# Performance work log

Hardware: AMD Instinct MI355X
Metric: run time of the kernel (lower is better)

## Reference

```python
import jax, jax.numpy as jnp
import numpy as np

B, U, D, SKIP = 2048, 1024, 1024, 24

def setup_inputs() -> dict:
    key = jax.random.key(0)
    ks = jax.random.split(key, 8)
    return {
        "inputs": jax.random.normal(ks[0], (B, D), dtype=jnp.float32),
        "h_tm1": jax.random.normal(ks[1], (B, 4 * U), dtype=jnp.float32),
        "c_tm1": jax.random.normal(ks[2], (B, U), dtype=jnp.float32),
        "step": jnp.zeros((B, 1), dtype=jnp.float32),
        "prev_h": jax.random.normal(ks[3], (B, U * SKIP), dtype=jnp.float32),
        "kernel": jax.random.normal(ks[4], (D, 4 * U), dtype=jnp.float32) * (1.0 / np.sqrt(D)),
        "recurrent_kernel": jax.random.normal(ks[5], (U, 4 * U), dtype=jnp.float32) * (1.0 / np.sqrt(U)),
        "kernel2": jax.random.normal(ks[6], (U, U), dtype=jnp.float32) * (1.0 / np.sqrt(U)),
        "bias": jnp.zeros((4 * U,), dtype=jnp.float32),
        "bias2": jnp.zeros((U,), dtype=jnp.float32),
        "s0": jnp.float32(0.5),
    }

def reference(inputs, h_tm1, c_tm1, step, prev_h, kernel, recurrent_kernel, kernel2, bias, bias2, s0):
    units = kernel2.shape[0]
    # split previous 'h' state into its four gate-history blocks [B, U] each
    h_parts = jnp.stack(jnp.split(h_tm1, 4, axis=1), axis=0)          # [4, B, U]
    rk = recurrent_kernel.reshape(units, 4, units)                     # [U, 4, U]
    # fused per-gate recurrent matmuls: r[g] = h_parts[g] @ recurrent_kernel[:, g*U:(g+1)*U]
    r = jnp.einsum('gbu,ugv->gbv', h_parts, rk)                        # [4, B, U]
    x = inputs @ kernel + bias                                         # [B, 4U]
    x_i, x_f, x_c, x_o = jnp.split(x, 4, axis=1)
    i = jax.nn.sigmoid(x_i + r[0])
    f = jax.nn.sigmoid(x_f + r[1])
    c = f * c_tm1 + i * jnp.tanh(x_c + r[2])
    o = jax.nn.sigmoid(x_o + r[3])
    h = o * jnp.tanh(c)
    new_h_skip = jax.nn.sigmoid(prev_h[:, :units] @ kernel2 + bias2)
    h = s0 * h + new_h_skip * (1 - s0)
    new_h_tm1 = jnp.concatenate([i, f, c, o], axis=1)
    new_prev_h = jnp.concatenate([prev_h[:, units:], h], axis=1)
    return (h, new_h_tm1, c, step + 1, new_prev_h)
```

## Files before the change

kernel.cpp:

```cpp
#include <hip/hip_runtime.h>
#include <hip/hip_bf16.h>
#include <stdint.h>

#define BB 2048
#define UU 1024
#define SKIPN 24

typedef __attribute__((ext_vector_type(8))) short short8;
typedef __attribute__((ext_vector_type(4))) float f32x4;
typedef __attribute__((ext_vector_type(4))) unsigned short ushort4_t;

static __device__ __forceinline__ float sigmoidf_(float x) {
    return 1.0f / (1.0f + __expf(-x));
}

static __device__ __forceinline__ void load_lds16(const void* g, void* l) {
    __builtin_amdgcn_global_load_lds((const __attribute__((address_space(1))) void*)g,
                                     (__attribute__((address_space(3))) void*)l, 16, 0, 0);
}

__global__ __launch_bounds__(256) void prep(
    const float* __restrict__ inputs, const float* __restrict__ h_tm1,
    const float* __restrict__ prev_h, const float* __restrict__ kernel,
    const float* __restrict__ rkernel, const float* __restrict__ kernel2,
    __hip_bfloat16* __restrict__ kt, __hip_bfloat16* __restrict__ rkt,
    __hip_bfloat16* __restrict__ k2t, __hip_bfloat16* __restrict__ xin,
    __hip_bfloat16* __restrict__ hb, __hip_bfloat16* __restrict__ ph0) {
    const int bid = blockIdx.x;
    if (bid < 9216) {
        __shared__ float tile[32][33];
        const float* src;
        __hip_bfloat16* dst;
        int C, local;
        if (bid < 4096)      { src = kernel;  dst = kt;  C = 4096; local = bid; }
        else if (bid < 8192) { src = rkernel; dst = rkt; C = 4096; local = bid - 4096; }
        else                 { src = kernel2; dst = k2t; C = 1024; local = bid - 8192; }
        const int xt = (C == 4096) ? 128 : 32;
        const int bc = (local % xt) * 32;
        const int br = (local / xt) * 32;
        const int tx = threadIdx.x & 31, ty = threadIdx.x >> 5;
#pragma unroll
        for (int i = 0; i < 32; i += 8)
            tile[ty + i][tx] = src[(size_t)(br + ty + i) * C + bc + tx];
        __syncthreads();
#pragma unroll
        for (int i = 0; i < 32; i += 8)
            dst[(size_t)(bc + ty + i) * 1024 + br + tx] = __float2bfloat16(tile[tx][ty + i]);
    } else {
        const int idx = (bid - 9216) * 256 + threadIdx.x;
        const float* src;
        __hip_bfloat16* dst;
        int off;
        if (idx < 524288) { dst = xin; off = idx; src = inputs + (size_t)off * 4; }
        else if (idx < 2621440) { off = idx - 524288; dst = hb; src = h_tm1 + (size_t)off * 4; }
        else {
            const int i = idx - 2621440;
            const int b = i >> 8, c4 = i & 255;
            off = i; dst = ph0;
            src = prev_h + (size_t)b * (UU * SKIPN) + c4 * 4;
        }
        const float4 v = *(const float4*)src;
        union { __hip_bfloat16 h[4]; ushort4_t u; } cv;
        cv.h[0] = __float2bfloat16(v.x);
        cv.h[1] = __float2bfloat16(v.y);
        cv.h[2] = __float2bfloat16(v.z);
        cv.h[3] = __float2bfloat16(v.w);
        *(ushort4_t*)(dst + (size_t)off * 4) = cv.u;
    }
}

__global__ __launch_bounds__(256) void mega3(
    const __hip_bfloat16* __restrict__ xin,
    const __hip_bfloat16* __restrict__ hb,
    const __hip_bfloat16* __restrict__ ph0,
    const __hip_bfloat16* __restrict__ kt,
    const __hip_bfloat16* __restrict__ rkt,
    const __hip_bfloat16* __restrict__ k2t,
    const float* __restrict__ prev_h, float* __restrict__ out_prev,
    float* __restrict__ pre) {
    const int bid = blockIdx.x;
    if (bid >= 640) {
        const int b = bid - 640;
        const float4* s = (const float4*)(prev_h + (size_t)b * 24576 + 1024);
        float4* d = (float4*)(out_prev + (size_t)b * 24576);
        for (int c = threadIdx.x; c < 5888; c += 256) d[c] = s[c];
        return;
    }
    const int gi = bid;
    const int g = gi % 5;
    const int t = gi / 5;
    const int v0 = (t & 7) * 128;
    const int b0 = (t >> 3) * 128;

    __shared__ short As[128 * 32];
    __shared__ short Bs[128 * 32];

    const int tid = threadIdx.x;
    const int lane = tid & 63;
    const int wid = tid >> 6;
    const int wrow = wid >> 1;
    const int wcol = wid & 1;

    const int srow = tid >> 2;
    const int sslot = tid & 3;
    const int kofs = ((sslot ^ (srow & 3)) << 3);
    char* dA = (char*)As + wid * 1024;
    char* dB = (char*)Bs + wid * 1024;

    const int l15 = lane & 15;
    const int hi = lane >> 4;
    const int rswB = ((hi ^ (l15 & 3)) << 4);

    f32x4 acc[4][4];
#pragma unroll
    for (int m = 0; m < 4; m++)
#pragma unroll
        for (int n = 0; n < 4; n++) acc[m][n] = (f32x4){0.f, 0.f, 0.f, 0.f};

    const __hip_bfloat16* A1;
    const __hip_bfloat16* W1;
    const __hip_bfloat16* A2 = nullptr;
    const __hip_bfloat16* W2 = nullptr;
    int lda1;
    if (g < 4) {
        A1 = xin; lda1 = 1024;
        W1 = kt + (size_t)g * 1048576;
        A2 = hb + (size_t)g * 1024;
        W2 = rkt + (size_t)g * 1048576;
    } else {
        A1 = ph0; lda1 = 1024;
        W1 = k2t;
    }

#define KSEG(AB, LDA, WB)                                                          \
    {                                                                              \
        const __hip_bfloat16* Ar0 = (AB) + (size_t)(b0 + srow) * (LDA) + kofs;     \
        const __hip_bfloat16* Ar1 = (AB) + (size_t)(b0 + 64 + srow) * (LDA) + kofs;\
        const __hip_bfloat16* Wr0 = (WB) + (size_t)(v0 + srow) * 1024 + kofs;      \
        const __hip_bfloat16* Wr1 = (WB) + (size_t)(v0 + 64 + srow) * 1024 + kofs; \
        for (int k0 = 0; k0 < 1024; k0 += 32) {                                    \
            load_lds16(Ar0 + k0, dA);                                              \
            load_lds16(Ar1 + k0, dA + 4096);                                       \
            load_lds16(Wr0 + k0, dB);                                              \
            load_lds16(Wr1 + k0, dB + 4096);                                       \
            __syncthreads();                                                       \
            short8 af[4], bfr[4];                                                  \
            _Pragma("unroll")                                                      \
            for (int m = 0; m < 4; m++)                                            \
                af[m] = *(const short8*)((char*)As + (wrow * 64 + m * 16 + l15) * 64 + rswB); \
            _Pragma("unroll")                                                      \
            for (int n = 0; n < 4; n++)                                            \
                bfr[n] = *(const short8*)((char*)Bs + (wcol * 64 + n * 16 + l15) * 64 + rswB); \
            _Pragma("unroll")                                                      \
            for (int m = 0; m < 4; m++)                                            \
                _Pragma("unroll")                                                  \
                for (int n = 0; n < 4; n++)                                        \
                    acc[m][n] = __builtin_amdgcn_mfma_f32_16x16x32_bf16(af[m], bfr[n], acc[m][n], 0, 0, 0); \
            __syncthreads();                                                       \
        }                                                                          \
    }

    KSEG(A1, lda1, W1);
    if (g < 4) KSEG(A2, 4096, W2);
#undef KSEG

    float* P = pre + (size_t)g * 2097152;
#pragma unroll
    for (int m = 0; m < 4; m++) {
#pragma unroll
        for (int n = 0; n < 4; n++) {
            const int col = v0 + wcol * 64 + n * 16 + l15;
            const int row = b0 + wrow * 64 + m * 16 + hi * 4;
#pragma unroll
            for (int r = 0; r < 4; r++)
                P[(size_t)(row + r) * 1024 + col] = acc[m][n][r];
        }
    }
}

__global__ __launch_bounds__(256) void epilogue2(
    const float* __restrict__ pre,
    const float* __restrict__ c_tm1, const float* __restrict__ bias,
    const float* __restrict__ bias2, const float* __restrict__ s0p,
    const float* __restrict__ step, float* __restrict__ out_h,
    float* __restrict__ out_ht, float* __restrict__ out_c,
    float* __restrict__ out_step, float* __restrict__ out_prev, int write_tail) {
    const int idx = blockIdx.x * 256 + threadIdx.x;
    const int b = idx >> 8;
    const int v = (idx & 255) * 4;
    const size_t bv = (size_t)b * 1024 + v;
    const float4 pi = *(const float4*)(pre + bv);
    const float4 pf = *(const float4*)(pre + 2097152 + bv);
    const float4 pc = *(const float4*)(pre + 4194304 + bv);
    const float4 po = *(const float4*)(pre + 6291456 + bv);
    const float4 ps = *(const float4*)(pre + 8388608 + bv);
    const float4 ct = *(const float4*)(c_tm1 + bv);
    const float4 bi = *(const float4*)(bias + v);
    const float4 bf_ = *(const float4*)(bias + 1024 + v);
    const float4 bc = *(const float4*)(bias + 2048 + v);
    const float4 bo = *(const float4*)(bias + 3072 + v);
    const float4 b2 = *(const float4*)(bias2 + v);
    const float s0 = s0p[0];

    float4 hv, iv4, fv4, cn4, ov4;
#pragma unroll
    for (int j = 0; j < 4; j++) {
        const float iv = sigmoidf_(((const float*)&pi)[j] + ((const float*)&bi)[j]);
        const float fv = sigmoidf_(((const float*)&pf)[j] + ((const float*)&bf_)[j]);
        const float cn = fv * ((const float*)&ct)[j] + iv * tanhf(((const float*)&pc)[j] + ((const float*)&bc)[j]);
        const float ov = sigmoidf_(((const float*)&po)[j] + ((const float*)&bo)[j]);
        const float sk = sigmoidf_(((const float*)&ps)[j] + ((const float*)&b2)[j]);
        ((float*)&hv)[j] = s0 * (ov * tanhf(cn)) + sk * (1.0f - s0);
        ((float*)&iv4)[j] = iv;
        ((float*)&fv4)[j] = fv;
        ((float*)&cn4)[j] = cn;
        ((float*)&ov4)[j] = ov;
    }
    *(float4*)(out_h + bv) = hv;
    *(float4*)(out_c + bv) = cn4;
    float* ht = out_ht + (size_t)b * 4096 + v;
    *(float4*)(ht) = iv4;
    *(float4*)(ht + 1024) = fv4;
    *(float4*)(ht + 2048) = cn4;
    *(float4*)(ht + 3072) = ov4;
    if (write_tail)
        *(float4*)(out_prev + (size_t)b * 24576 + 23552 + v) = hv;
    if (idx < 2048) out_step[idx] = step[idx] + 1.0f;
}

__global__ __launch_bounds__(256) void shift_only(
    const float* __restrict__ prev_h, const float* __restrict__ out_h,
    float* __restrict__ out_prev) {
    const int b = blockIdx.x;
    float4* d = (float4*)(out_prev + (size_t)b * 24576);
    const float4* s1 = (const float4*)(prev_h + (size_t)b * 24576 + 1024);
    const float4* s2 = (const float4*)(out_h + (size_t)b * 1024);
    for (int c = threadIdx.x; c < 6144; c += 256)
        d[c] = (c < 5888) ? s1[c] : s2[c - 5888];
}

extern "C" void kernel_launch(void* const* d_in, const int* in_sizes, int n_in,
                              void* d_out, int out_size, void* d_ws, size_t ws_size,
                              hipStream_t stream) {
    (void)in_sizes; (void)n_in; (void)out_size;
    const float* inputs = (const float*)d_in[0];
    const float* h_tm1 = (const float*)d_in[1];
    const float* c_tm1 = (const float*)d_in[2];
    const float* step = (const float*)d_in[3];
    const float* prev_h = (const float*)d_in[4];
    const float* kernel = (const float*)d_in[5];
    const float* rkernel = (const float*)d_in[6];
    const float* kernel2 = (const float*)d_in[7];
    const float* bias = (const float*)d_in[8];
    const float* bias2 = (const float*)d_in[9];
    const float* s0 = (const float*)d_in[10];

    float* out = (float*)d_out;
    float* out_h = out;
    float* out_ht = out + 2097152;
    float* out_c = out + 10485760;
    float* out_step = out + 12582912;
    float* out_prev = out + 12584960;

    const size_t NEED = 44040192 + 41943040;
    const int fits = (ws_size >= NEED);
    char* scr = fits ? (char*)d_ws : (char*)out_prev;
    __hip_bfloat16* kt = (__hip_bfloat16*)(scr + 0);
    __hip_bfloat16* rkt = (__hip_bfloat16*)(scr + 8388608);
    __hip_bfloat16* k2t = (__hip_bfloat16*)(scr + 16777216);
    __hip_bfloat16* xin = (__hip_bfloat16*)(scr + 18874368);
    __hip_bfloat16* hb = (__hip_bfloat16*)(scr + 23068672);
    __hip_bfloat16* ph0 = (__hip_bfloat16*)(scr + 39845888);
    float* pre = (float*)(scr + 44040192);

    prep<<<21504, 256, 0, stream>>>(inputs, h_tm1, prev_h, kernel, rkernel, kernel2,
                                    kt, rkt, k2t, xin, hb, ph0);
    if (fits) {
        mega3<<<2688, 256, 0, stream>>>(xin, hb, ph0, kt, rkt, k2t, prev_h, out_prev, pre);
        epilogue2<<<2048, 256, 0, stream>>>(pre, c_tm1, bias, bias2, s0, step,
                                            out_h, out_ht, out_c, out_step, out_prev, 1);
    } else {
        mega3<<<640, 256, 0, stream>>>(xin, hb, ph0, kt, rkt, k2t, prev_h, out_prev, pre);
        epilogue2<<<2048, 256, 0, stream>>>(pre, c_tm1, bias, bias2, s0, step,
                                            out_h, out_ht, out_c, out_step, out_prev, 0);
        shift_only<<<2048, 256, 0, stream>>>(prev_h, out_h, out_prev);
    }
}
```

Measured before the change: 196.8 us.

## Double-buffer LDS tiles in GEMM kernel and use nontemporal copy for prev_h shift

The GEMM main loop now uses two LDS buffers, issuing the next k-tile's global-to-LDS loads before computing on the current tile. It replaces __syncthreads with explicit vmcnt/lgkmcnt waits and raw s_barrier so memory latency can overlap with MFMA work. The prev_h shift-copy blocks switch to unrolled nontemporal loads and stores to avoid polluting the cache. LDS use doubles, which may reduce occupancy, and the hand-placed waitcnts are fragile.

```diff
diff --git a/kernel.cpp b/kernel.cpp
--- a/kernel.cpp
+++ b/kernel.cpp
@@ -17,6 +17,13 @@
 static __device__ __forceinline__ void load_lds16(const void* g, void* l) {
     __builtin_amdgcn_global_load_lds((const __attribute__((address_space(1))) void*)g,
                                      (__attribute__((address_space(3))) void*)l, 16, 0, 0);
+}
+
+static __device__ __forceinline__ f32x4 ntl(const f32x4* p) {
+    return __builtin_nontemporal_load(p);
+}
+static __device__ __forceinline__ void nts(f32x4* p, f32x4 v) {
+    __builtin_nontemporal_store(v, p);
 }
 
 __global__ __launch_bounds__(256) void prep(
@@ -69,7 +76,7 @@
     }
 }
 
-__global__ __launch_bounds__(256) void mega3(
+__global__ __launch_bounds__(256) void mega4(
     const __hip_bfloat16* __restrict__ xin,
     const __hip_bfloat16* __restrict__ hb,
     const __hip_bfloat16* __restrict__ ph0,
@@ -81,9 +88,29 @@
     const int bid = blockIdx.x;
     if (bid >= 640) {
         const int b = bid - 640;
-        const float4* s = (const float4*)(prev_h + (size_t)b * 24576 + 1024);
-        float4* d = (float4*)(out_prev + (size_t)b * 24576);
-        for (int c = threadIdx.x; c < 5888; c += 256) d[c] = s[c];
+        const f32x4* s = (const f32x4*)(prev_h + (size_t)b * 24576 + 1024);
+        f32x4* d = (f32x4*)(out_prev + (size_t)b * 24576);
+        int c = threadIdx.x;
+#pragma unroll 1
+        for (int it = 0; it < 5; ++it) {
+            f32x4 v0 = ntl(s + c);
+            f32x4 v1 = ntl(s + c + 256);
+            f32x4 v2 = ntl(s + c + 512);
+            f32x4 v3 = ntl(s + c + 768);
+            nts(d + c, v0);
+            nts(d + c + 256, v1);
+            nts(d + c + 512, v2);
+            nts(d + c + 768, v3);
+            c += 1024;
+        }
+        {
+            f32x4 v0 = ntl(s + c);
+            f32x4 v1 = ntl(s + c + 256);
+            f32x4 v2 = ntl(s + c + 512);
+            nts(d + c, v0);
+            nts(d + c + 256, v1);
+            nts(d + c + 512, v2);
+        }
         return;
     }
     const int gi = bid;
@@ -92,8 +119,8 @@
     const int v0 = (t & 7) * 128;
     const int b0 = (t >> 3) * 128;
 
-    __shared__ short As[128 * 32];
-    __shared__ short Bs[128 * 32];
+    __shared__ char As[2 * 8192];
+    __shared__ char Bs[2 * 8192];
 
     const int tid = threadIdx.x;
     const int lane = tid & 63;
@@ -104,8 +131,7 @@
     const int srow = tid >> 2;
     const int sslot = tid & 3;
     const int kofs = ((sslot ^ (srow & 3)) << 3);
-    char* dA = (char*)As + wid * 1024;
-    char* dB = (char*)Bs + wid * 1024;
+    const int ldst = wid * 1024;
 
     const int l15 = lane & 15;
     const int hi = lane >> 4;
@@ -132,31 +158,52 @@
         W1 = k2t;
     }
 
+#define BARRIER() asm volatile("s_barrier" ::: "memory")
+#define WAITV(N) asm volatile("s_waitcnt vmcnt(" #N ")" ::: "memory")
+#define WAITL0() asm volatile("s_waitcnt lgkmcnt(0)" ::: "memory")
+
 #define KSEG(AB, LDA, WB)                                                          \
     {                                                                              \
         const __hip_bfloat16* Ar0 = (AB) + (size_t)(b0 + srow) * (LDA) + kofs;     \
         const __hip_bfloat16* Ar1 = (AB) + (size_t)(b0 + 64 + srow) * (LDA) + kofs;\
         const __hip_bfloat16* Wr0 = (WB) + (size_t)(v0 + srow) * 1024 + kofs;      \
         const __hip_bfloat16* Wr1 = (WB) + (size_t)(v0 + 64 + srow) * 1024 + kofs; \
-        for (int k0 = 0; k0 < 1024; k0 += 32) {                                    \
-            load_lds16(Ar0 + k0, dA);                                              \
-            load_lds16(Ar1 + k0, dA + 4096);                                       \
-            load_lds16(Wr0 + k0, dB);                                              \
-            load_lds16(Wr1 + k0, dB + 4096);                                       \
-            __syncthreads();                                                       \
+        load_lds16(Ar0, As + ldst);                                                \
+        load_lds16(Ar1, As + ldst + 4096);                                         \
+        load_lds16(Wr0, Bs + ldst);                                                \
+        load_lds16(Wr1, Bs + ldst + 4096);                                         \
+        _Pragma("unroll 2")                                                        \
+        for (int t_ = 0; t_ < 32; ++t_) {                                          \
+            const int cur = t_ & 1;                                                \
+            char* Ac = As + cur * 8192;                                            \
+            char* Bc = Bs + cur * 8192;                                            \
+            if (t_ < 31) {                                                         \
+                const int kn = (t_ + 1) * 32;                                      \
+                char* An = As + (cur ^ 1) * 8192 + ldst;                           \
+                char* Bn = Bs + (cur ^ 1) * 8192 + ldst;                           \
+                load_lds16(Ar0 + kn, An);                                          \
+                load_lds16(Ar1 + kn, An + 4096);                                   \
+                load_lds16(Wr0 + kn, Bn);                                          \
+                load_lds16(Wr1 + kn, Bn + 4096);                                   \
+                WAITV(4);                                                          \
+            } else {                                                               \
+                WAITV(0);                                                          \
+            }                                                                      \
+            BARRIER();                                                             \
             short8 af[4], bfr[4];                                                  \
             _Pragma("unroll")                                                      \
             for (int m = 0; m < 4; m++)                                            \
-                af[m] = *(const short8*)((char*)As + (wrow * 64 + m * 16 + l15) * 64 + rswB); \
+                af[m] = *(const short8*)(Ac + (wrow * 64 + m * 16 + l15) * 64 + rswB); \
             _Pragma("unroll")                                                      \
             for (int n = 0; n < 4; n++)                                            \
-                bfr[n] = *(const short8*)((char*)Bs + (wcol * 64 + n * 16 + l15) * 64 + rswB); \
+                bfr[n] = *(const short8*)(Bc + (wcol * 64 + n * 16 + l15) * 64 + rswB); \
             _Pragma("unroll")                                                      \
             for (int m = 0; m < 4; m++)                                            \
                 _Pragma("unroll")                                                  \
                 for (int n = 0; n < 4; n++)                                        \
                     acc[m][n] = __builtin_amdgcn_mfma_f32_16x16x32_bf16(af[m], bfr[n], acc[m][n], 0, 0, 0); \
-            __syncthreads();                                                       \
+            WAITL0();                                                              \
+            BARRIER();                                                             \
         }                                                                          \
     }
 
@@ -176,6 +223,9 @@
                 P[(size_t)(row + r) * 1024 + col] = acc[m][n][r];
         }
     }
+#undef BARRIER
+#undef WAITV
+#undef WAITL0
 }
 
 __global__ __launch_bounds__(256) void epilogue2(
@@ -276,11 +326,11 @@
     prep<<<21504, 256, 0, stream>>>(inputs, h_tm1, prev_h, kernel, rkernel, kernel2,
                                     kt, rkt, k2t, xin, hb, ph0);
     if (fits) {
-        mega3<<<2688, 256, 0, stream>>>(xin, hb, ph0, kt, rkt, k2t, prev_h, out_prev, pre);
+        mega4<<<2688, 256, 0, stream>>>(xin, hb, ph0, kt, rkt, k2t, prev_h, out_prev, pre);
         epilogue2<<<2048, 256, 0, stream>>>(pre, c_tm1, bias, bias2, s0, step,
                                             out_h, out_ht, out_c, out_step, out_prev, 1);
     } else {
-        mega3<<<640, 256, 0, stream>>>(xin, hb, ph0, kt, rkt, k2t, prev_h, out_prev, pre);
+        mega4<<<640, 256, 0, stream>>>(xin, hb, ph0, kt, rkt, k2t, prev_h, out_prev, pre);
         epilogue2<<<2048, 256, 0, stream>>>(pre, c_tm1, bias, bias2, s0, step,
                                             out_h, out_ht, out_c, out_step, out_prev, 0);
         shift_only<<<2048, 256, 0, stream>>>(prev_h, out_h, out_prev);
```

Measured after the change: 173.8 us. -11.7%, faster.
